# Optimization experiments

Hardware: AMD Instinct MI355X
Metric: run time of the kernel (lower is better)

Reference implementation:

```python
import jax, jax.numpy as jnp
import numpy as np

D_MODEL, N_LAYERS, NUM_CLASSES = 768, 4, 10
D_INNER = 2 * D_MODEL          # expand_factor=2
D_STATE = 16
D_CONV = 4
DT_RANK = (D_MODEL + 15) // 16  # ceil(d_model/16) = 48
B, L = 8, 2048
EPS = 1e-5


def setup_inputs() -> dict:
    key = jax.random.key(0)
    ks = jax.random.split(key, 16)
    s = 0.02
    inp = {
        'x': jax.random.normal(ks[0], (B, L, D_MODEL), jnp.float32),
        'labels': jax.random.randint(ks[1], (B,), 0, NUM_CLASSES, jnp.int64),
        # stacked per-layer params
        'in_proj_w': jax.random.normal(ks[2], (N_LAYERS, 2 * D_INNER, D_MODEL), jnp.float32) * s,
        'conv_w': jax.random.normal(ks[3], (N_LAYERS, D_INNER, 1, D_CONV), jnp.float32) * s,
        'conv_b': jnp.zeros((N_LAYERS, D_INNER), jnp.float32),
        'x_proj_w': jax.random.normal(ks[4], (N_LAYERS, DT_RANK + 2 * D_STATE, D_INNER), jnp.float32) * s,
        'dt_w': jax.random.normal(ks[5], (N_LAYERS, D_INNER, DT_RANK), jnp.float32) * s,
        'dt_b': jax.random.uniform(ks[6], (N_LAYERS, D_INNER), jnp.float32, -4.0, -2.0),
        'A_log': jnp.broadcast_to(jnp.log(jnp.arange(1, D_STATE + 1, dtype=jnp.float32)),
                                  (N_LAYERS, D_INNER, D_STATE)).copy(),
        'D_param': jnp.ones((N_LAYERS, D_INNER), jnp.float32),
        'out_proj_w': jax.random.normal(ks[7], (N_LAYERS, D_MODEL, D_INNER), jnp.float32) * s,
        'norm_w': jnp.ones((N_LAYERS, D_MODEL), jnp.float32),
        'normf_w': jnp.ones((D_MODEL,), jnp.float32),
        'cls_w': jax.random.normal(ks[8], (NUM_CLASSES, D_MODEL), jnp.float32) * s,
        'cls_b': jnp.zeros((NUM_CLASSES,), jnp.float32),
    }
    return inp


def rmsnorm(x, w):
    return x * jax.lax.rsqrt(jnp.mean(x * x, axis=-1, keepdims=True) + EPS) * w


def causal_dw_conv1d(x, w, b):
    # x: (B, L, ED), w: (ED, 1, K) depthwise, causal left padding
    y = jax.lax.conv_general_dilated(
        x.swapaxes(1, 2), w, window_strides=(1,), padding=[(D_CONV - 1, 0)],
        feature_group_count=D_INNER, dimension_numbers=('NCH', 'OIH', 'NCH'))
    return (y + b[:, None]).swapaxes(1, 2)


def selective_scan(xin, delta, Bm, Cm, A, Dp):
    # xin/delta: (B,L,ED), Bm/Cm: (B,L,N), A: (ED,N), Dp: (ED,)
    def step(h, t):
        d_t, B_t, C_t, x_t = t                      # (B,ED),(B,N),(B,N),(B,ED)
        dA = jnp.exp(d_t[..., None] * A)            # (B,ED,N)
        dBx = (d_t * x_t)[..., None] * B_t[:, None, :]
        h = dA * h + dBx
        y = jnp.einsum('ben,bn->be', h, C_t)
        return h, y

    h0 = jnp.zeros((xin.shape[0], D_INNER, D_STATE), xin.dtype)
    xs = (delta.swapaxes(0, 1), Bm.swapaxes(0, 1), Cm.swapaxes(0, 1), xin.swapaxes(0, 1))
    _, ys = jax.lax.scan(step, h0, xs)              # ys: (L,B,ED)
    return ys.swapaxes(0, 1) + xin * Dp


def mamba_block(x, in_w, cw, cb, xw, dtw, dtb, A_log, Dp, ow):
    xz = jnp.einsum('bld,ed->ble', x, in_w)         # (B,L,2*ED)
    xin, z = jnp.split(xz, 2, axis=-1)
    xin = jax.nn.silu(causal_dw_conv1d(xin, cw, cb))
    dbc = jnp.einsum('ble,fe->blf', xin, xw)
    delta_r = dbc[..., :DT_RANK]
    Bm = dbc[..., DT_RANK:DT_RANK + D_STATE]
    Cm = dbc[..., DT_RANK + D_STATE:]
    delta = jax.nn.softplus(jnp.einsum('blr,er->ble', delta_r, dtw) + dtb)
    A = -jnp.exp(A_log)
    y = selective_scan(xin, delta, Bm, Cm, A, Dp)
    y = y * jax.nn.silu(z)
    return jnp.einsum('ble,de->bld', y, ow)


def forward(x, labels, in_proj_w, conv_w, conv_b, x_proj_w, dt_w, dt_b,
            A_log, D_param, out_proj_w, norm_w, normf_w, cls_w, cls_b):
    h = x
    for i in range(N_LAYERS):
        h = h + mamba_block(rmsnorm(h, norm_w[i]), in_proj_w[i], conv_w[i], conv_b[i],
                            x_proj_w[i], dt_w[i], dt_b[i], A_log[i], D_param[i], out_proj_w[i])
    h = rmsnorm(h, normf_w)
    pooled = jnp.mean(h, axis=1)                    # (B, d_model)
    logits = pooled @ cls_w.T + cls_b               # (B, num_classes)
    logp = jax.nn.log_softmax(logits, axis=-1)
    loss = -jnp.mean(jnp.take_along_axis(logp, labels[:, None], axis=-1))
    return logits, loss


def reference(x, labels, in_proj_w, conv_w, conv_b, x_proj_w, dt_w, dt_b,
              A_log, D_param, out_proj_w, norm_w, normf_w, cls_w, cls_b):
    return forward(x, labels, in_proj_w, conv_w, conv_b, x_proj_w, dt_w, dt_b,
                   A_log, D_param, out_proj_w, norm_w, normf_w, cls_w, cls_b)
```

## Files before the change

### kernel.cpp

```cpp
#include <hip/hip_runtime.h>
#include <hip/hip_bf16.h>
#include <math.h>

#define MTOK 16384
#define DM   768
#define DI   1536
#define DS   16
#define RNK  48
#define LSEQ 2048
#define NBATCH 8
#define EPSV 1e-5f
#define CHK  16
#define CLEN (LSEQ / CHK)
#define BM 128
#define BN 128
#define BK 32
#define KSPLIT 8
#define EPS_STRIDE 72

typedef __hip_bfloat16 bf16;
typedef __attribute__((ext_vector_type(8))) short short8;
typedef __attribute__((ext_vector_type(4))) float floatx4;

__device__ __forceinline__ float b2f(bf16 v){ return __bfloat162float(v); }
__device__ __forceinline__ bf16  f2b(float v){ return __float2bfloat16(v); }
__device__ __forceinline__ float u2f(unsigned short u){
    union { unsigned int i; float f; } v; v.i = ((unsigned int)u) << 16; return v.f;
}
__device__ __forceinline__ float silu_f(float x){
    return x * __builtin_amdgcn_rcpf(1.f + __expf(-x));
}
__device__ __forceinline__ void gload_lds16(const void* g, void* l) {
    __builtin_amdgcn_global_load_lds(
        (const __attribute__((address_space(1))) void*)g,
        (__attribute__((address_space(3))) void*)l, 16, 0, 0);
}

__global__ __launch_bounds__(256) void cvt_kernel(
    const float* __restrict__ x, bf16* __restrict__ h, int n)
{
    int i = blockIdx.x * 256 + threadIdx.x;
    if (i < n) h[i] = f2b(x[i]);
}

__global__ __launch_bounds__(256) void rmsnorm_kernel(
    const bf16* __restrict__ in, const float* __restrict__ w,
    bf16* __restrict__ out, float* __restrict__ rs_out)
{
    int row = blockIdx.x;
    const bf16* r = in + (size_t)row * DM;
    float v0 = b2f(r[threadIdx.x]);
    float v1 = b2f(r[threadIdx.x + 256]);
    float v2 = b2f(r[threadIdx.x + 512]);
    float s = v0*v0 + v1*v1 + v2*v2;
    for (int o = 32; o > 0; o >>= 1) s += __shfl_down(s, o, 64);
    __shared__ float red[4];
    if ((threadIdx.x & 63) == 0) red[threadIdx.x >> 6] = s;
    __syncthreads();
    float rs = rsqrtf((red[0]+red[1]+red[2]+red[3]) * (1.f/DM) + EPSV);
    if (rs_out && threadIdx.x == 0) rs_out[row] = rs;
    if (out) {
        out[(size_t)row*DM + threadIdx.x]       = f2b(v0 * rs * w[threadIdx.x]);
        out[(size_t)row*DM + threadIdx.x + 256] = f2b(v1 * rs * w[threadIdx.x + 256]);
        out[(size_t)row*DM + threadIdx.x + 512] = f2b(v2 * rs * w[threadIdx.x + 512]);
    }
}

template<int MODE, int CONVA>
__global__ __launch_bounds__(256) void mgemm(
    const short* __restrict__ A, int lda,
    const short* __restrict__ W, int ldw,
    bf16* __restrict__ C, int ldc,
    int M, int N, int K,
    const float* __restrict__ cw, const float* __restrict__ cb,
    int ksteps_per_split)
{
    __shared__ __attribute__((aligned(16))) short As[BM*BK];
    __shared__ __attribute__((aligned(16))) short Bs[BN*BK];
    const int bm = blockIdx.y * BM;
    const int bn = blockIdx.x * BN;
    const int tid = threadIdx.x;
    const int wave = tid >> 6;
    const int lane = tid & 63;
    const int wm = (wave & 1) * 64;
    const int wn = (wave >> 1) * 64;
    const int r15 = lane & 15;
    const int quad = lane >> 4;

    int kbeg = 0, kend = K;
    if (MODE == 4) {
        kbeg = blockIdx.z * ksteps_per_split * BK;
        kend = kbeg + ksteps_per_split * BK;
        if (kend > K) kend = K;
    }

    const int srow = wave*32 + (lane >> 2);
    const int swz = (lane & 3) ^ ((lane >> 2) & 3);
    int wr0 = bn + srow;      if (wr0 >= N) wr0 = N - 1;
    int wr1 = bn + srow + 16; if (wr1 >= N) wr1 = N - 1;

    floatx4 acc[4][4];
    const floatx4 zero = {0.f, 0.f, 0.f, 0.f};
    #pragma unroll
    for (int i = 0; i < 4; i++)
        #pragma unroll
        for (int j = 0; j < 4; j++) acc[i][j] = zero;

    const int kk = tid & 31;
    const int tg = tid >> 5;
    const int sA = CONVA ? quad : (quad ^ (r15 & 3));
    const int sB = quad ^ (r15 & 3);

    for (int k0 = kbeg; k0 < kend; k0 += BK) {
        if (CONVA) {
            int e = k0 + kk;
            float c0 = cw[e*4+0], c1 = cw[e*4+1], c2 = cw[e*4+2], c3 = cw[e*4+3];
            float cbe = cb[e];
            int g0 = bm + tg*16;
            const unsigned short* xp = (const unsigned short*)A + (size_t)g0 * lda + e;
            float p0 = 0.f, p1 = 0.f, p2 = 0.f;
            if ((g0 & (LSEQ-1)) != 0) {
                p0 = u2f(xp[-(ptrdiff_t)3*lda]);
                p1 = u2f(xp[-(ptrdiff_t)2*lda]);
                p2 = u2f(xp[-(ptrdiff_t)1*lda]);
            }
            #pragma unroll
            for (int i = 0; i < 16; i++) {
                float xt = u2f(xp[(size_t)i * lda]);
                float xv = silu_f(cbe + c0*p0 + c1*p1 + c2*p2 + c3*xt);
                p0 = p1; p1 = p2; p2 = xt;
                bf16 t = f2b(xv);
                As[(tg*16 + i)*BK + kk] = *(short*)&t;
            }
        } else {
            gload_lds16(A + (size_t)(bm + srow)      * lda + k0 + swz*8, &As[(wave*32)*BK]);
            gload_lds16(A + (size_t)(bm + srow + 16) * lda + k0 + swz*8, &As[(wave*32 + 16)*BK]);
        }
        gload_lds16(W + (size_t)wr0 * ldw + k0 + swz*8, &Bs[(wave*32)*BK]);
        gload_lds16(W + (size_t)wr1 * ldw + k0 + swz*8, &Bs[(wave*32 + 16)*BK]);
        __syncthreads();

        short8 af[4], bfr[4];
        #pragma unroll
        for (int i = 0; i < 4; i++) af[i]  = *(const short8*)&As[(wm + i*16 + r15)*BK + sA*8];
        #pragma unroll
        for (int i = 0; i < 4; i++) bfr[i] = *(const short8*)&Bs[(wn + i*16 + r15)*BK + sB*8];
        #pragma unroll
        for (int mt = 0; mt < 4; mt++)
            #pragma unroll
            for (int nt = 0; nt < 4; nt++)
                acc[mt][nt] = __builtin_amdgcn_mfma_f32_16x16x32_bf16(
                    af[mt], bfr[nt], acc[mt][nt], 0, 0, 0);
        __syncthreads();
    }

    if (MODE == 4) {
        float* Cf = (float*)C;
        #pragma unroll
        for (int nt = 0; nt < 4; nt++) {
            int n = bn + wn + nt*16 + r15;
            if (n >= N) continue;
            #pragma unroll
            for (int mt = 0; mt < 4; mt++)
                #pragma unroll
                for (int reg = 0; reg < 4; reg++) {
                    int m = bm + wm + mt*16 + quad*4 + reg;
                    atomicAdd(&Cf[(size_t)m * ldc + n], acc[mt][nt][reg]);
                }
        }
        return;
    }

    short* ep = ((wave & 2) ? Bs : As) + (wave & 1) * 1152;
    const int lr = lane >> 2;
    const int lc = lane & 3;
    #pragma unroll
    for (int mt = 0; mt < 4; mt++) {
        #pragma unroll
        for (int nt = 0; nt < 4; nt++)
            #pragma unroll
            for (int reg = 0; reg < 4; reg++) {
                bf16 t = f2b(acc[mt][nt][reg]);
                ep[(quad*4 + reg)*EPS_STRIDE + nt*16 + r15] = *(short*)&t;
            }
        short8 v0 = *(const short8*)&ep[lr*EPS_STRIDE + lc*16];
        short8 v1 = *(const short8*)&ep[lr*EPS_STRIDE + lc*16 + 8];
        int gm = bm + wm + mt*16 + lr;
        int gn = bn + wn + lc*16;
        if (gn < N) {
            bf16* cp = C + (size_t)gm * ldc + gn;
            if (MODE == 0) {
                *(short8*)cp       = v0;
                *(short8*)(cp + 8) = v1;
            } else {
                short8 c0 = *(const short8*)cp;
                short8 c1 = *(const short8*)(cp + 8);
                short8 o0, o1;
                #pragma unroll
                for (int j = 0; j < 8; j++) {
                    float cv0 = u2f((unsigned short)c0[j]);
                    float av0 = u2f((unsigned short)v0[j]);
                    float cv1 = u2f((unsigned short)c1[j]);
                    float av1 = u2f((unsigned short)v1[j]);
                    float r0 = (MODE == 2) ? (cv0 + av0) : (cv0 * silu_f(av0));
                    float r1 = (MODE == 2) ? (cv1 + av1) : (cv1 * silu_f(av1));
                    bf16 t0 = f2b(r0), t1 = f2b(r1);
                    o0[j] = *(short*)&t0;
                    o1[j] = *(short*)&t1;
                }
                *(short8*)cp       = o0;
                *(short8*)(cp + 8) = o1;
            }
        }
    }
}

template<int PASS>
__global__ __launch_bounds__(256) void scan_pass_kernel(
    bf16* __restrict__ xy,
    const bf16* __restrict__ dbc,
    const float* __restrict__ A_log,
    const float* __restrict__ Dp,
    const float* __restrict__ dtw,
    const float* __restrict__ dtb,
    const float* __restrict__ cw,
    const float* __restrict__ cb,
    float* __restrict__ hst,
    float* __restrict__ Ssum,
    unsigned short* __restrict__ bound)
{
    int e = (blockIdx.x % (DI/256)) * 256 + threadIdx.x;
    int b = (blockIdx.x / (DI/256)) & (NBATCH - 1);
    int c = blockIdx.x / ((DI/256) * NBATCH);
    int t0 = c * CLEN;

    float w[RNK];
    #pragma unroll
    for (int r = 0; r < RNK; r++) w[r] = dtw[e*RNK + r];
    float a[DS];
    #pragma unroll
    for (int n = 0; n < DS; n++) a[n] = -__expf(A_log[e*DS + n]);
    float c0 = cw[e*4+0], c1 = cw[e*4+1], c2 = cw[e*4+2], c3 = cw[e*4+3];
    float cbe = cb[e], dtbe = dtb[e], dpe = Dp[e];

    size_t sidx = ((size_t)(b*DI) + e) * CHK + c;
    float hh[DS];
    if (PASS == 1) {
        #pragma unroll
        for (int n = 0; n < DS; n++) hh[n] = 0.f;
    } else {
        #pragma unroll
        for (int n = 0; n < DS; n++) hh[n] = hst[sidx*DS + n];
    }

    unsigned short* xrow = (unsigned short*)(xy + ((size_t)(b*LSEQ) + t0) * DI + e);
    const unsigned short* drow = (const unsigned short*)(dbc + ((size_t)(b*LSEQ) + t0) * 80);

    unsigned short r0, r1, r2;
    if (PASS == 1) {
        if (c == 0) { r0 = 0; r1 = 0; r2 = 0; }
        else {
            r0 = xrow[-(ptrdiff_t)3*DI];
            r1 = xrow[-(ptrdiff_t)2*DI];
            r2 = xrow[-(ptrdiff_t)1*DI];
        }
        bound[sidx*4+0] = r0; bound[sidx*4+1] = r1; bound[sidx*4+2] = r2;
    } else {
        r0 = bound[sidx*4+0]; r1 = bound[sidx*4+1]; r2 = bound[sidx*4+2];
    }
    float p0 = u2f(r0), p1 = u2f(r1), p2 = u2f(r2);

    float S = 0.f;
    for (int t = 0; t < CLEN; t++) {
        float xt = u2f(xrow[(size_t)t * DI]);
        float xv = silu_f(cbe + c0*p0 + c1*p1 + c2*p2 + c3*xt);
        p0 = p1; p1 = p2; p2 = xt;

        uint4 q[5];
        const uint4* d4 = (const uint4*)(drow + (size_t)t * 80);
        #pragma unroll
        for (int i = 0; i < 5; i++) q[i] = d4[i];
        uint4 q2[5];
        #pragma unroll
        for (int i = 0; i < 5; i++) q2[i] = d4[5 + i];
        const unsigned short* ds = (const unsigned short*)q;
        const unsigned short* ds2 = (const unsigned short*)q2;

        float acc = dtbe;
        #pragma unroll
        for (int r = 0; r < RNK; r++) acc += w[r] * u2f(ds[r]);
        float d = (acc > 20.f) ? acc : __logf(1.f + __expf(acc));
        float dx = d * xv;
        #pragma unroll
        for (int n = 0; n < DS; n++)
            hh[n] = __expf(d * a[n]) * hh[n] + dx * u2f(ds[RNK + n]);

        if (PASS == 1) {
            S += d;
        } else {
            float y = xv * dpe;
            #pragma unroll
            for (int n = 0; n < DS; n++) y += hh[n] * u2f(ds2[n]);
            bf16 yb = f2b(y);
            xrow[(size_t)t * DI] = *(unsigned short*)&yb;
        }
    }
    if (PASS == 1) {
        #pragma unroll
        for (int n = 0; n < DS; n++) hst[sidx*DS + n] = hh[n];
        Ssum[sidx] = S;
    }
}

__global__ __launch_bounds__(256) void scan_combine_kernel(
    float* __restrict__ hst, const float* __restrict__ Ssum,
    const float* __restrict__ A_log)
{
    int tid = blockIdx.x * 256 + threadIdx.x;
    int n = tid & 15;
    int bee = tid >> 4;
    int e = bee % DI;
    float a = -__expf(A_log[e*DS + n]);
    float run = 0.f;
    for (int c = 0; c < CHK; c++) {
        size_t idx = ((size_t)bee * CHK + c) * DS + n;
        float tmp = hst[idx];
        hst[idx] = run;
        run = tmp + __expf(a * Ssum[(size_t)bee*CHK + c]) * run;
    }
}

__global__ __launch_bounds__(128) void pool_kernel(
    const bf16* __restrict__ h, const float* __restrict__ rs,
    const float* __restrict__ wf, float* __restrict__ pooled)
{
    int b = blockIdx.x, dc = blockIdx.y, tc = blockIdx.z;
    int d = dc * 128 + threadIdx.x;
    float s = 0.f;
    int t0 = tc * 128;
    for (int t = t0; t < t0 + 128; t++) {
        int row = b * LSEQ + t;
        s += b2f(h[(size_t)row * DM + d]) * rs[row];
    }
    atomicAdd(&pooled[b * DM + d], s * wf[d] * (1.f / LSEQ));
}

__global__ __launch_bounds__(128) void head_kernel(
    const float* __restrict__ pooled, const float* __restrict__ cls_w,
    const float* __restrict__ cls_b, const int* __restrict__ labels,
    float* __restrict__ out)
{
    __shared__ float lg[80];
    int tid = threadIdx.x;
    if (tid < 80) {
        int b = tid / 10, c = tid % 10;
        float s = cls_b[c];
        for (int d = 0; d < DM; d++) s += pooled[b * DM + d] * cls_w[c * DM + d];
        lg[tid] = s;
    }
    __syncthreads();
    if (tid == 0) {
        float loss = 0.f;
        for (int b = 0; b < NBATCH; b++) {
            float mx = -1e30f;
            for (int c = 0; c < 10; c++) mx = fmaxf(mx, lg[b*10+c]);
            float se = 0.f;
            for (int c = 0; c < 10; c++) se += expf(lg[b*10+c] - mx);
            float lse = mx + logf(se);
            loss -= (lg[b*10 + labels[b]] - lse);
            for (int c = 0; c < 10; c++) out[b*10+c] = lg[b*10+c];
        }
        out[80] = loss / NBATCH;
    }
}

extern "C" void kernel_launch(void* const* d_in, const int* in_sizes, int n_in,
                              void* d_out, int out_size, void* d_ws, size_t ws_size,
                              hipStream_t stream) {
    const float* x          = (const float*)d_in[0];
    const int*   labels     = (const int*)d_in[1];
    const float* in_proj_w  = (const float*)d_in[2];
    const float* conv_w     = (const float*)d_in[3];
    const float* conv_b     = (const float*)d_in[4];
    const float* x_proj_w   = (const float*)d_in[5];
    const float* dt_w       = (const float*)d_in[6];
    const float* dt_b       = (const float*)d_in[7];
    const float* A_log      = (const float*)d_in[8];
    const float* D_param    = (const float*)d_in[9];
    const float* out_proj_w = (const float*)d_in[10];
    const float* norm_w     = (const float*)d_in[11];
    const float* normf_w    = (const float*)d_in[12];
    const float* cls_w      = (const float*)d_in[13];
    const float* cls_b      = (const float*)d_in[14];
    float* out = (float*)d_out;

    char* p = (char*)d_ws;
    bf16* h   = (bf16*)p;                 p += (size_t)MTOK * DM * 2;
    bf16* xn  = (bf16*)p;                 p += (size_t)MTOK * DM * 2;
    bf16* xy  = (bf16*)p;                 p += (size_t)MTOK * DI * 2;
    bf16* dbc = (bf16*)p;                 p += (size_t)MTOK * 80 * 2;
    float* dbcf = (float*)p;              p += (size_t)MTOK * 80 * 4;
    float* hst = (float*)p;               p += (size_t)NBATCH*DI*CHK*DS*4;
    float* Ssum = (float*)p;              p += (size_t)NBATCH*DI*CHK*4;
    unsigned short* bound = (unsigned short*)p; p += (size_t)NBATCH*DI*CHK*4*2;
    float* rsb    = (float*)p;            p += (size_t)MTOK * 4;
    float* pooled = (float*)p;            p += NBATCH * DM * 4;
    short* inw_b = (short*)p;             p += (size_t)2*DI*DM * 2;
    short* xw_b  = (short*)p;             p += (size_t)80*DI * 2;
    short* ow_b  = (short*)p;             p += (size_t)DM*DI * 2;

    cvt_kernel<<<(MTOK * DM) / 256, 256, 0, stream>>>(x, h, MTOK * DM);
    hipMemsetAsync(pooled, 0, NBATCH * DM * sizeof(float), stream);

    int scan_grid = (DI/256) * NBATCH * CHK;

    for (int l = 0; l < 4; l++) {
        const float* inw = in_proj_w + (size_t)l * 2 * DI * DM;
        const float* cwl = conv_w + (size_t)l * DI * 4;
        const float* cbl = conv_b + (size_t)l * DI;
        const float* xwl = x_proj_w + (size_t)l * (RNK + 2*DS) * DI;
        const float* dwl = dt_w + (size_t)l * DI * RNK;
        const float* dbl = dt_b + (size_t)l * DI;
        const float* All = A_log + (size_t)l * DI * DS;
        const float* Dpl = D_param + (size_t)l * DI;
        const float* owl = out_proj_w + (size_t)l * DM * DI;

        cvt_kernel<<<(2*DI*DM)/256, 256, 0, stream>>>(inw, (bf16*)inw_b, 2*DI*DM);
        cvt_kernel<<<(80*DI)/256, 256, 0, stream>>>(xwl, (bf16*)xw_b, 80*DI);
        cvt_kernel<<<(DM*DI)/256, 256, 0, stream>>>(owl, (bf16*)ow_b, DM*DI);

        rmsnorm_kernel<<<MTOK, 256, 0, stream>>>(h, norm_w + (size_t)l * DM, xn, nullptr);

        hipMemsetAsync(dbcf, 0, (size_t)MTOK * 80 * sizeof(float), stream);

        mgemm<0,0><<<dim3(DI/BN, MTOK/BM), 256, 0, stream>>>(
            (const short*)xn, DM, inw_b, DM, xy, DI, MTOK, DI, DM, nullptr, nullptr, 0);

        mgemm<4,1><<<dim3(1, MTOK/BM, KSPLIT), 256, 0, stream>>>(
            (const short*)xy, DI, xw_b, DI, (bf16*)dbcf, 80, MTOK, 80, DI,
            cwl, cbl, (DI/BK)/KSPLIT);
        cvt_kernel<<<(MTOK*80)/256, 256, 0, stream>>>(dbcf, dbc, MTOK*80);

        scan_pass_kernel<1><<<scan_grid, 256, 0, stream>>>(
            xy, dbc, All, Dpl, dwl, dbl, cwl, cbl, hst, Ssum, bound);
        scan_combine_kernel<<<(NBATCH*DI*DS)/256, 256, 0, stream>>>(hst, Ssum, All);
        scan_pass_kernel<2><<<scan_grid, 256, 0, stream>>>(
            xy, dbc, All, Dpl, dwl, dbl, cwl, cbl, hst, Ssum, bound);

        mgemm<3,0><<<dim3(DI/BN, MTOK/BM), 256, 0, stream>>>(
            (const short*)xn, DM, inw_b + (size_t)DI*DM, DM, xy, DI, MTOK, DI, DM,
            nullptr, nullptr, 0);

        mgemm<2,0><<<dim3(DM/BN, MTOK/BM), 256, 0, stream>>>(
            (const short*)xy, DI, ow_b, DI, h, DM, MTOK, DM, DI, nullptr, nullptr, 0);
    }

    rmsnorm_kernel<<<MTOK, 256, 0, stream>>>(h, normf_w, nullptr, rsb);
    pool_kernel<<<dim3(NBATCH, DM/128, LSEQ/128), 128, 0, stream>>>(h, rsb, normf_w, pooled);
    head_kernel<<<1, 128, 0, stream>>>(pooled, cls_w, cls_b, labels, out);
}
```

Measured before the change: 1.318 ms.

## Merge in_proj GEMMs, compute delta via MFMA GEMM, fuse gating into scan

Adds a second code path, used when the workspace is large enough. It runs one in_proj GEMM that writes x and z together into a 3072-wide buffer. The dt projection becomes a padded bf16 GEMM with a bias-plus-softplus epilogue, instead of 48-rank dot products repeated per timestep in both scan passes. The silu(z) gating moves into the second scan pass, which removes the separate z GEMM. In exchange it adds a materialized delta buffer, extra memory traffic, padding conversions and a large workspace requirement.

```diff
diff --git a/kernel.cpp b/kernel.cpp
--- a/kernel.cpp
+++ b/kernel.cpp
@@ -41,6 +41,16 @@
 {
     int i = blockIdx.x * 256 + threadIdx.x;
     if (i < n) h[i] = f2b(x[i]);
+}
+
+__global__ __launch_bounds__(256) void cvt_pad_kernel(
+    const float* __restrict__ x, bf16* __restrict__ o, int sc, int dc, int n)
+{
+    int i = blockIdx.x * 256 + threadIdx.x;
+    if (i >= n) return;
+    int col = i % dc;
+    int row = i / dc;
+    o[i] = (col < sc) ? f2b(x[(size_t)row * sc + col]) : f2b(0.f);
 }
 
 __global__ __launch_bounds__(256) void rmsnorm_kernel(
@@ -73,6 +83,7 @@
     bf16* __restrict__ C, int ldc,
     int M, int N, int K,
     const float* __restrict__ cw, const float* __restrict__ cb,
+    const float* __restrict__ ep_bias,
     int ksteps_per_split)
 {
     __shared__ __attribute__((aligned(16))) short As[BM*BK];
@@ -177,19 +188,30 @@
     #pragma unroll
     for (int mt = 0; mt < 4; mt++) {
         #pragma unroll
-        for (int nt = 0; nt < 4; nt++)
+        for (int nt = 0; nt < 4; nt++) {
+            float bias = 0.f;
+            if (MODE == 1) {
+                int n = bn + wn + nt*16 + r15;
+                bias = ep_bias[n < N ? n : N-1];
+            }
             #pragma unroll
             for (int reg = 0; reg < 4; reg++) {
-                bf16 t = f2b(acc[mt][nt][reg]);
+                float v = acc[mt][nt][reg];
+                if (MODE == 1) {
+                    v += bias;
+                    v = (v > 20.f) ? v : __logf(1.f + __expf(v));
+                }
+                bf16 t = f2b(v);
                 ep[(quad*4 + reg)*EPS_STRIDE + nt*16 + r15] = *(short*)&t;
             }
+        }
         short8 v0 = *(const short8*)&ep[lr*EPS_STRIDE + lc*16];
         short8 v1 = *(const short8*)&ep[lr*EPS_STRIDE + lc*16 + 8];
         int gm = bm + wm + mt*16 + lr;
         int gn = bn + wn + lc*16;
         if (gn < N) {
             bf16* cp = C + (size_t)gm * ldc + gn;
-            if (MODE == 0) {
+            if (MODE == 0 || MODE == 1) {
                 *(short8*)cp       = v0;
                 *(short8*)(cp + 8) = v1;
             } else {
@@ -216,17 +238,102 @@
 }
 
 template<int PASS>
+__global__ __launch_bounds__(256) void scan_fused_kernel(
+    bf16* __restrict__ xz,
+    const bf16* __restrict__ delta,
+    const bf16* __restrict__ dbc,
+    const float* __restrict__ A_log, const float* __restrict__ Dp,
+    const float* __restrict__ cw, const float* __restrict__ cb,
+    float* __restrict__ hst, float* __restrict__ Ssum,
+    unsigned short* __restrict__ bound)
+{
+    int e = (blockIdx.x % (DI/256)) * 256 + threadIdx.x;
+    int b = (blockIdx.x / (DI/256)) & (NBATCH - 1);
+    int c = blockIdx.x / ((DI/256) * NBATCH);
+    int t0 = c * CLEN;
+
+    float a[DS];
+    #pragma unroll
+    for (int n = 0; n < DS; n++) a[n] = -__expf(A_log[e*DS + n]);
+    float c0 = cw[e*4+0], c1 = cw[e*4+1], c2 = cw[e*4+2], c3 = cw[e*4+3];
+    float cbe = cb[e], dpe = Dp[e];
+
+    size_t sidx = ((size_t)(b*DI) + e) * CHK + c;
+    float hh[DS];
+    if (PASS == 1) {
+        #pragma unroll
+        for (int n = 0; n < DS; n++) hh[n] = 0.f;
+    } else {
+        #pragma unroll
+        for (int n = 0; n < DS; n++) hh[n] = hst[sidx*DS + n];
+    }
+
+    unsigned short* xrow = (unsigned short*)xz + ((size_t)(b*LSEQ) + t0) * 3072 + e;
+    const unsigned short* drow = (const unsigned short*)delta + ((size_t)(b*LSEQ) + t0) * DI + e;
+    const unsigned short* brow = (const unsigned short*)dbc + ((size_t)(b*LSEQ) + t0) * 128;
+
+    unsigned short r0, r1, r2;
+    if (PASS == 1) {
+        if (c == 0) { r0 = 0; r1 = 0; r2 = 0; }
+        else {
+            r0 = xrow[-(ptrdiff_t)3*3072];
+            r1 = xrow[-(ptrdiff_t)2*3072];
+            r2 = xrow[-(ptrdiff_t)1*3072];
+        }
+        bound[sidx*4+0] = r0; bound[sidx*4+1] = r1; bound[sidx*4+2] = r2;
+    } else {
+        r0 = bound[sidx*4+0]; r1 = bound[sidx*4+1]; r2 = bound[sidx*4+2];
+    }
+    float p0 = u2f(r0), p1 = u2f(r1), p2 = u2f(r2);
+
+    float S = 0.f;
+    for (int t = 0; t < CLEN; t++) {
+        float xt = u2f(xrow[(size_t)t * 3072]);
+        float xv = silu_f(cbe + c0*p0 + c1*p1 + c2*p2 + c3*xt);
+        p0 = p1; p1 = p2; p2 = xt;
+
+        float d = u2f(drow[(size_t)t * DI]);
+
+        uint4 qb[2];
+        qb[0] = *(const uint4*)(brow + (size_t)t*128 + 48);
+        qb[1] = *(const uint4*)(brow + (size_t)t*128 + 56);
+        const unsigned short* Bv = (const unsigned short*)qb;
+
+        float dx = d * xv;
+        #pragma unroll
+        for (int n = 0; n < DS; n++)
+            hh[n] = __expf(d * a[n]) * hh[n] + dx * u2f(Bv[n]);
+
+        if (PASS == 1) {
+            S += d;
+        } else {
+            uint4 qc[2];
+            qc[0] = *(const uint4*)(brow + (size_t)t*128 + 64);
+            qc[1] = *(const uint4*)(brow + (size_t)t*128 + 72);
+            const unsigned short* Cv = (const unsigned short*)qc;
+            float y = xv * dpe;
+            #pragma unroll
+            for (int n = 0; n < DS; n++) y += hh[n] * u2f(Cv[n]);
+            float zv = u2f(xrow[(size_t)t * 3072 + DI]);
+            y *= silu_f(zv);
+            bf16 yb = f2b(y);
+            xrow[(size_t)t * 3072] = *(unsigned short*)&yb;
+        }
+    }
+    if (PASS == 1) {
+        #pragma unroll
+        for (int n = 0; n < DS; n++) hst[sidx*DS + n] = hh[n];
+        Ssum[sidx] = S;
+    }
+}
+
+template<int PASS>
 __global__ __launch_bounds__(256) void scan_pass_kernel(
-    bf16* __restrict__ xy,
-    const bf16* __restrict__ dbc,
-    const float* __restrict__ A_log,
-    const float* __restrict__ Dp,
-    const float* __restrict__ dtw,
-    const float* __restrict__ dtb,
-    const float* __restrict__ cw,
-    const float* __restrict__ cb,
-    float* __restrict__ hst,
-    float* __restrict__ Ssum,
+    bf16* __restrict__ xy, const bf16* __restrict__ dbc,
+    const float* __restrict__ A_log, const float* __restrict__ Dp,
+    const float* __restrict__ dtw, const float* __restrict__ dtb,
+    const float* __restrict__ cw, const float* __restrict__ cb,
+    float* __restrict__ hst, float* __restrict__ Ssum,
     unsigned short* __restrict__ bound)
 {
     int e = (blockIdx.x % (DI/256)) * 256 + threadIdx.x;
@@ -394,6 +501,80 @@
     const float* cls_b      = (const float*)d_in[14];
     float* out = (float*)d_out;
 
+    const size_t FULL_NEED = 234000000ull;
+    int scan_grid = (DI/256) * NBATCH * CHK;
+
+    if (ws_size >= FULL_NEED) {
+        char* p = (char*)d_ws;
+        bf16* h     = (bf16*)p;  p += (size_t)MTOK * DM * 2;
+        bf16* xn    = (bf16*)p;  p += (size_t)MTOK * DM * 2;
+        bf16* xz    = (bf16*)p;  p += (size_t)MTOK * 3072 * 2;
+        bf16* delta = (bf16*)p;  p += (size_t)MTOK * DI * 2;
+        bf16* dbc   = (bf16*)p;  p += (size_t)MTOK * 128 * 2;
+        float* dbcf = (float*)p; p += (size_t)MTOK * 80 * 4;
+        float* hst  = (float*)p; p += (size_t)NBATCH*DI*CHK*DS*4;
+        float* Ssum = (float*)p; p += (size_t)NBATCH*DI*CHK*4;
+        unsigned short* bound = (unsigned short*)p; p += (size_t)NBATCH*DI*CHK*4*2;
+        float* rsb    = (float*)p; p += (size_t)MTOK * 4;
+        float* pooled = (float*)p; p += NBATCH * DM * 4;
+        short* inw_b = (short*)p;  p += (size_t)2*DI*DM * 2;
+        short* xw_b  = (short*)p;  p += (size_t)80*DI * 2;
+        short* ow_b  = (short*)p;  p += (size_t)DM*DI * 2;
+        short* dtwp  = (short*)p;  p += (size_t)DI*128 * 2;
+
+        cvt_kernel<<<(MTOK * DM) / 256, 256, 0, stream>>>(x, h, MTOK * DM);
+        hipMemsetAsync(pooled, 0, NBATCH * DM * sizeof(float), stream);
+
+        for (int l = 0; l < 4; l++) {
+            const float* inw = in_proj_w + (size_t)l * 2 * DI * DM;
+            const float* cwl = conv_w + (size_t)l * DI * 4;
+            const float* cbl = conv_b + (size_t)l * DI;
+            const float* xwl = x_proj_w + (size_t)l * (RNK + 2*DS) * DI;
+            const float* dwl = dt_w + (size_t)l * DI * RNK;
+            const float* dbl = dt_b + (size_t)l * DI;
+            const float* All = A_log + (size_t)l * DI * DS;
+            const float* Dpl = D_param + (size_t)l * DI;
+            const float* owl = out_proj_w + (size_t)l * DM * DI;
+
+            cvt_kernel<<<(2*DI*DM)/256, 256, 0, stream>>>(inw, (bf16*)inw_b, 2*DI*DM);
+            cvt_kernel<<<(80*DI)/256, 256, 0, stream>>>(xwl, (bf16*)xw_b, 80*DI);
+            cvt_kernel<<<(DM*DI)/256, 256, 0, stream>>>(owl, (bf16*)ow_b, DM*DI);
+            cvt_pad_kernel<<<(DI*128)/256, 256, 0, stream>>>(dwl, (bf16*)dtwp, RNK, 128, DI*128);
+
+            rmsnorm_kernel<<<MTOK, 256, 0, stream>>>(h, norm_w + (size_t)l * DM, xn, nullptr);
+
+            mgemm<0,0><<<dim3(3072/BN, MTOK/BM), 256, 0, stream>>>(
+                (const short*)xn, DM, inw_b, DM, xz, 3072, MTOK, 3072, DM,
+                nullptr, nullptr, nullptr, 0);
+
+            hipMemsetAsync(dbcf, 0, (size_t)MTOK * 80 * sizeof(float), stream);
+
+            mgemm<4,1><<<dim3(1, MTOK/BM, KSPLIT), 256, 0, stream>>>(
+                (const short*)xz, 3072, xw_b, DI, (bf16*)dbcf, 80, MTOK, 80, DI,
+                cwl, cbl, nullptr, (DI/BK)/KSPLIT);
+            cvt_pad_kernel<<<(MTOK*128)/256, 256, 0, stream>>>(dbcf, dbc, 80, 128, MTOK*128);
+
+            mgemm<1,0><<<dim3(DI/BN, MTOK/BM), 256, 0, stream>>>(
+                (const short*)dbc, 128, dtwp, 128, delta, DI, MTOK, DI, 128,
+                nullptr, nullptr, dbl, 0);
+
+            scan_fused_kernel<1><<<scan_grid, 256, 0, stream>>>(
+                xz, delta, dbc, All, Dpl, cwl, cbl, hst, Ssum, bound);
+            scan_combine_kernel<<<(NBATCH*DI*DS)/256, 256, 0, stream>>>(hst, Ssum, All);
+            scan_fused_kernel<2><<<scan_grid, 256, 0, stream>>>(
+                xz, delta, dbc, All, Dpl, cwl, cbl, hst, Ssum, bound);
+
+            mgemm<2,0><<<dim3(DM/BN, MTOK/BM), 256, 0, stream>>>(
+                (const short*)xz, 3072, ow_b, DI, h, DM, MTOK, DM, DI,
+                nullptr, nullptr, nullptr, 0);
+        }
+
+        rmsnorm_kernel<<<MTOK, 256, 0, stream>>>(h, normf_w, nullptr, rsb);
+        pool_kernel<<<dim3(NBATCH, DM/128, LSEQ/128), 128, 0, stream>>>(h, rsb, normf_w, pooled);
+        head_kernel<<<1, 128, 0, stream>>>(pooled, cls_w, cls_b, labels, out);
+        return;
+    }
+
     char* p = (char*)d_ws;
     bf16* h   = (bf16*)p;                 p += (size_t)MTOK * DM * 2;
     bf16* xn  = (bf16*)p;                 p += (size_t)MTOK * DM * 2;
@@ -412,8 +593,6 @@
     cvt_kernel<<<(MTOK * DM) / 256, 256, 0, stream>>>(x, h, MTOK * DM);
     hipMemsetAsync(pooled, 0, NBATCH * DM * sizeof(float), stream);
 
-    int scan_grid = (DI/256) * NBATCH * CHK;
-
     for (int l = 0; l < 4; l++) {
         const float* inw = in_proj_w + (size_t)l * 2 * DI * DM;
         const float* cwl = conv_w + (size_t)l * DI * 4;
@@ -431,14 +610,14 @@
 
         rmsnorm_kernel<<<MTOK, 256, 0, stream>>>(h, norm_w + (size_t)l * DM, xn, nullptr);
 
+        mgemm<0,0><<<dim3(DI/BN, MTOK/BM), 256, 0, stream>>>(
+            (const short*)xn, DM, inw_b, DM, xy, DI, MTOK, DI, DM,
+            nullptr, nullptr, nullptr, 0);
+
         hipMemsetAsync(dbcf, 0, (size_t)MTOK * 80 * sizeof(float), stream);
-
-        mgemm<0,0><<<dim3(DI/BN, MTOK/BM), 256, 0, stream>>>(
-            (const short*)xn, DM, inw_b, DM, xy, DI, MTOK, DI, DM, nullptr, nullptr, 0);
-
         mgemm<4,1><<<dim3(1, MTOK/BM, KSPLIT), 256, 0, stream>>>(
             (const short*)xy, DI, xw_b, DI, (bf16*)dbcf, 80, MTOK, 80, DI,
-            cwl, cbl, (DI/BK)/KSPLIT);
+            cwl, cbl, nullptr, (DI/BK)/KSPLIT);
         cvt_kernel<<<(MTOK*80)/256, 256, 0, stream>>>(dbcf, dbc, MTOK*80);
 
         scan_pass_kernel<1><<<scan_grid, 256, 0, stream>>>(
@@ -449,10 +628,11 @@
 
         mgemm<3,0><<<dim3(DI/BN, MTOK/BM), 256, 0, stream>>>(
             (const short*)xn, DM, inw_b + (size_t)DI*DM, DM, xy, DI, MTOK, DI, DM,
-            nullptr, nullptr, 0);
+            nullptr, nullptr, nullptr, 0);
 
         mgemm<2,0><<<dim3(DM/BN, MTOK/BM), 256, 0, stream>>>(
-            (const short*)xy, DI, ow_b, DI, h, DM, MTOK, DM, DI, nullptr, nullptr, 0);
+            (const short*)xy, DI, ow_b, DI, h, DM, MTOK, DM, DI,
+            nullptr, nullptr, nullptr, 0);
     }
 
     rmsnorm_kernel<<<MTOK, 256, 0, stream>>>(h, normf_w, nullptr, rsb);
```

After: 2.486 ms. 1.89x slower.
